# Optimization experiments

Measured on AMD Instinct MI355X. Metric: run time of the kernel, lower is better.

The kernel has to match this reference:

```python
import jax, jax.numpy as jnp
import numpy as np
from jax import lax

EPS = 1e-5

def _conv(x, w, b, stride):
    y = lax.conv_general_dilated(x, w, window_strides=(stride, stride), padding='VALID',
                                 dimension_numbers=('NCHW', 'OIHW', 'NCHW'))
    return y + b[None, :, None, None]

def _upsample_zero(x, s):
    B, C, H, W = x.shape
    z = jnp.zeros((B, C, H * s, W * s), dtype=x.dtype)
    return z.at[:, :, ::s, ::s].set(x)

def setup_inputs() -> dict:
    key = jax.random.key(0)
    ks = jax.random.split(key, 12)
    B, C, H, W = 512, 3, 128, 128
    FLAT = 3 * 65 * 65  # 12675 per the shape chain
    sc = lambda fan_in: 1.0 / np.sqrt(fan_in)
    return {
        'x': jax.random.normal(ks[0], (B, C, H, W), dtype=jnp.float32),
        'bn_gamma': jnp.ones((C,), jnp.float32),
        'bn_beta': jnp.zeros((C,), jnp.float32),
        'w1': jax.random.normal(ks[1], (3, 3, 5, 5), jnp.float32) * sc(3 * 25),
        'b1': jax.random.normal(ks[2], (3,), jnp.float32) * 0.01,
        'w2': jax.random.normal(ks[3], (3, 3, 5, 5), jnp.float32) * sc(3 * 25),
        'b2': jax.random.normal(ks[4], (3,), jnp.float32) * 0.01,
        'fc1_w': jax.random.normal(ks[5], (128, FLAT), jnp.float32) * sc(FLAT),
        'fc1_b': jnp.zeros((128,), jnp.float32),
        'fc2_w': jax.random.normal(ks[6], (10, 128), jnp.float32) * sc(128),
        'fc2_b': jnpp if False else jnp.zeros((10,), jnp.float32),
    }

def reference(x, bn_gamma, bn_beta, w1, b1, w2, b2, fc1_w, fc1_b, fc2_w, fc2_b):
    # BatchNorm1d over active sites (= all original pixels; zero-pad sites are inactive)
    mean = x.mean(axis=(0, 2, 3))
    var = ((x - mean[None, :, None, None]) ** 2).mean(axis=(0, 2, 3))  # biased, as torch BN
    xn = (x - mean[None, :, None, None]) * lax.rsqrt(var + EPS)[None, :, None, None]
    xn = xn * bn_gamma[None, :, None, None] + bn_beta[None, :, None, None]
    # SparseZeroPad2d(1) -> [B,3,130,130]
    h = jnp.pad(xn, ((0, 0), (0, 0), (1, 1), (1, 1)))
    # cv1 (k5,s5) -> [B,3,26,26]; SparseScale2d(5) -> zeros interleaved [B,3,130,130]
    h = _upsample_zero(_conv(h, w1, b1, 5), 5)
    h = jax.nn.relu(h)
    # cv2 (k5,s5) -> [B,3,26,26]; scale -> [B,3,130,130]
    h = _upsample_zero(_conv(h, w2, b2, 5), 5)
    h = jax.nn.relu(h)
    # SparseMaxPool2d(2,2) -> [B,3,65,65]; features >= 0 so dense pool matches sparse pool
    h = lax.reduce_window(h, -jnp.inf, lax.max, (1, 1, 2, 2), (1, 1, 2, 2), 'VALID')
    # flatten -> dropout(eval=identity) -> fc1 -> relu -> fc2 -> log_softmax
    f = h.reshape(h.shape[0], -1)
    f = jax.nn.relu(f @ fc1_w.T + fc1_b)
    logits = f @ fc2_w.T + fc2_b
    return jax.nn.log_softmax(logits, axis=1)
```

## Files before the change

kernel.cpp:

```cpp
#include <hip/hip_runtime.h>

#define BN_EPS 1e-5f

typedef short short8 __attribute__((ext_vector_type(8)));
typedef float f32x4 __attribute__((ext_vector_type(4)));
typedef unsigned short ushort;

__device__ inline ushort f2bf(float f) {
  unsigned int u = __float_as_uint(f);
  u += 0x7FFFu + ((u >> 16) & 1u);
  return (ushort)(u >> 16);
}


#define NPOS 346112
#define LR 136
#define NW 6656

__global__ __launch_bounds__(256) void k_convwave(
    const float* __restrict__ x,
    const float* __restrict__ w1g,
    float* __restrict__ S,
    float* __restrict__ psumA)
{
  __shared__ float lds[4][10 * LR];
  const int tid = threadIdx.x;
  const int lane = tid & 63;
  const int w = tid >> 6;
  float* sx = lds[w];

  const int widx = blockIdx.x * 4 + w;
  const int b = widx / 39;
  const int r39 = widx - b * 39;
  const int c = r39 / 13;
  const int band = r39 - c * 13;
  const int cu = __builtin_amdgcn_readfirstlane(c);

  if (lane < 10) sx[lane * LR + 3] = 0.f;
  else if (lane < 20) sx[(lane - 10) * LR + 132] = 0.f;

  const float* xc = x + ((size_t)b * 3 + c) * 16384;
  const int rbase = 10 * band - 1;
  float s = 0.f, q = 0.f;
  #pragma unroll
  for (int u = 0; u < 5; u++) {
    int v = lane + 64 * u;
    int j = v >> 5;
    int col4 = (v & 31) << 2;
    int r = rbase + j;
    float4 a4 = {0.f, 0.f, 0.f, 0.f};
    if (r >= 0 && r < 128) a4 = *(const float4*)(xc + r * 128 + col4);
    *(float4*)(&sx[j * LR + col4 + 4]) = a4;
    s += (a4.x + a4.y) + (a4.z + a4.w);
    q += (a4.x * a4.x + a4.y * a4.y) + (a4.z * a4.z + a4.w * a4.w);
  }

  const int ol = lane >> 5;
  const int ox = lane & 31;
  if (ox < 26) {
    const float* base = &sx[(5 * ol) * LR + 5 * ox + 3];
    const float* wk = w1g + cu * 25;
    float a0 = 0.f, a1 = 0.f, a2 = 0.f;
    #pragma unroll
    for (int ky = 0; ky < 5; ky++) {
      #pragma unroll
      for (int kx = 0; kx < 5; kx++) {
        float vv = base[ky * LR + kx];
        a0 += wk[ky * 5 + kx] * vv;
        a1 += wk[75 + ky * 5 + kx] * vv;
        a2 += wk[150 + ky * 5 + kx] * vv;
      }
    }
    int oy = 2 * band + ol;
    size_t gp = (size_t)b * 676 + oy * 26 + ox;
    S[(size_t)(c * 3 + 0) * NPOS + gp] = a0;
    S[(size_t)(c * 3 + 1) * NPOS + gp] = a1;
    S[(size_t)(c * 3 + 2) * NPOS + gp] = a2;
  }

  #pragma unroll
  for (int off = 32; off; off >>= 1) {
    s += __shfl_down(s, off);
    q += __shfl_down(q, off);
  }
  if (lane == 0) {
    int pos = b * 13 + band;
    psumA[(size_t)c * NW + pos] = s;
    psumA[(size_t)(3 + c) * NW + pos] = q;
  }
}

__global__ __launch_bounds__(1024) void k_reduce(const float* __restrict__ psumA,
                                                 float* __restrict__ stats) {
  const int sidx = blockIdx.x;
  const float* src = psumA + (size_t)sidx * NW;
  float acc = 0.f;
  for (int i = threadIdx.x; i < NW; i += 1024) acc += src[i];
  #pragma unroll
  for (int off = 32; off; off >>= 1) acc += __shfl_down(acc, off);
  __shared__ float r[16];
  if ((threadIdx.x & 63) == 0) r[threadIdx.x >> 6] = acc;
  __syncthreads();
  if (threadIdx.x == 0) {
    float t = 0.f;
    #pragma unroll
    for (int i = 0; i < 16; i++) t += r[i];
    stats[sidx] = t;
  }
}

__device__ inline float gval(const float* __restrict__ row, int k) {
  if (k >= 2028) return 0.f;
  int c = k / 676;
  int rem = k - c * 676;
  int oy = rem / 26, ox = rem - oy * 26;
  int col = c * 4225 + ((5 * oy) >> 1) * 65 + ((5 * ox) >> 1);
  return row[col];
}

__global__ __launch_bounds__(256) void k_gather(const float* __restrict__ fc1_w,
                                                ushort* __restrict__ WgtB,
                                                ushort* __restrict__ featB) {
  int gid = blockIdx.x * 256 + threadIdx.x;
  if (gid < 10240)
    featB[(size_t)(gid / 20) * 2048 + 2028 + (gid % 20)] = 0;
  int l = gid & 63;
  int n = ((gid >> 12) << 4) + (l & 15);
  int kbase = (((gid >> 6) & 63) << 5) + ((l >> 4) << 3);
  const float* row = fc1_w + n * 12675;
  uint4 o;
  unsigned int w[4];
  #pragma unroll
  for (int i = 0; i < 4; i++) {
    ushort lo = f2bf(gval(row, kbase + 2 * i));
    ushort hi = f2bf(gval(row, kbase + 2 * i + 1));
    w[i] = (unsigned int)lo | ((unsigned int)hi << 16);
  }
  o.x = w[0]; o.y = w[1]; o.z = w[2]; o.w = w[3];
  ((uint4*)WgtB)[gid] = o;
}

__global__ __launch_bounds__(256) void k_combine(
    const float* __restrict__ S,
    const float* __restrict__ stats,
    const float* __restrict__ gamma, const float* __restrict__ beta,
    const float* __restrict__ w1, const float* __restrict__ b1,
    const float* __restrict__ w2, const float* __restrict__ b2,
    ushort* __restrict__ featB)
{
  __shared__ float s_w1[225];
  __shared__ float s_w2[9];
  __shared__ float s_scale[3], s_shift[3], s_b1[3], s_b2[3];
  __shared__ float s_T[9][9];
  const int tid = threadIdx.x;
  if (tid < 225) s_w1[tid] = w1[tid];
  if (tid < 9) s_w2[tid] = w2[tid * 25];
  if (tid < 3) {
    const float N = 512.f * 128.f * 128.f;
    float mean = stats[tid] / N;
    float var = stats[3 + tid] / N - mean * mean;
    float sc = gamma[tid] * rsqrtf(var + BN_EPS);
    s_scale[tid] = sc;
    s_shift[tid] = beta[tid] - mean * sc;
    s_b1[tid] = b1[tid];
    s_b2[tid] = b2[tid];
  }
  __syncthreads();
  if (tid < 81) {
    int cls = tid / 9, oc = tid - (tid / 9) * 9;
    int rcl = cls / 3, ccl = cls - rcl * 3;
    int o = oc / 3, c = oc - o * 3;
    int ky0 = (rcl == 0) ? 1 : 0, ky1 = (rcl == 2) ? 3 : 4;
    int kx0 = (ccl == 0) ? 1 : 0, kx1 = (ccl == 2) ? 3 : 4;
    float t = 0.f;
    for (int ky = ky0; ky <= ky1; ky++)
      for (int kx = kx0; kx <= kx1; kx++)
        t += s_w1[o * 75 + c * 25 + ky * 5 + kx];
    s_T[cls][oc] = t;
  }
  __syncthreads();

  int gpos = blockIdx.x * 256 + tid;
  int b = gpos / 676;
  int pos = gpos - b * 676;
  int oy = pos / 26, ox = pos - oy * 26;
  int rcl = (oy == 0) ? 0 : ((oy == 25) ? 2 : 1);
  int ccl = (ox == 0) ? 0 : ((ox == 25) ? 2 : 1);
  int cls = rcl * 3 + ccl;

  float h[3];
  #pragma unroll
  for (int o = 0; o < 3; o++) {
    float a = s_b1[o];
    #pragma unroll
    for (int c = 0; c < 3; c++) {
      a += s_scale[c] * S[(size_t)(c * 3 + o) * NPOS + gpos];
      a += s_shift[c] * s_T[cls][o * 3 + c];
    }
    h[o] = fmaxf(a, 0.f);
  }
  ushort* fb = featB + (size_t)b * 2048;
  #pragma unroll
  for (int o = 0; o < 3; o++) {
    float v = s_b2[o] + s_w2[3 * o] * h[0] + s_w2[3 * o + 1] * h[1] + s_w2[3 * o + 2] * h[2];
    fb[o * 676 + pos] = f2bf(fmaxf(v, 0.f));
  }
}

__global__ __launch_bounds__(512) void k_fc(
    const ushort* __restrict__ featB,
    const ushort* __restrict__ WgtB,
    const float* __restrict__ fc1_b,
    const float* __restrict__ fc2_w, const float* __restrict__ fc2_b,
    float* __restrict__ out)
{
  __shared__ float s_f[16][132];
  __shared__ float s_lg[16][10];
  const int tid = threadIdx.x;
  const int lane = tid & 63;
  const int t = tid >> 6;
  const int m0 = blockIdx.x * 16;

  const ushort* aptr = featB + (size_t)(m0 + (lane & 15)) * 2048 + ((lane >> 4) << 3);
  const ushort* bptr = WgtB + ((size_t)t * 4096 + lane) * 8;

  f32x4 acc = {0.f, 0.f, 0.f, 0.f};
  #pragma unroll 4
  for (int kk = 0; kk < 64; kk++) {
    short8 a = *(const short8*)(aptr + kk * 32);
    short8 bfr = *(const short8*)(bptr + kk * 512);
    acc = __builtin_amdgcn_mfma_f32_16x16x32_bf16(a, bfr, acc, 0, 0, 0);
  }
  {
    int n = t * 16 + (lane & 15);
    float bias = fc1_b[n];
    int mb = (lane >> 4) << 2;
    #pragma unroll
    for (int r = 0; r < 4; r++)
      s_f[mb + r][n] = fmaxf(acc[r] + bias, 0.f);
  }
  __syncthreads();

  if (tid < 160) {
    int m = tid & 15, q = tid >> 4;
    const float* wr = fc2_w + q * 128;
    float a2 = fc2_b[q];
    #pragma unroll 8
    for (int n = 0; n < 128; n++) a2 += wr[n] * s_f[m][n];
    s_lg[m][q] = a2;
  }
  __syncthreads();

  if (tid < 16) {
    float mx = s_lg[tid][0];
    #pragma unroll
    for (int q = 1; q < 10; q++) mx = fmaxf(mx, s_lg[tid][q]);
    float se = 0.f;
    #pragma unroll
    for (int q = 0; q < 10; q++) se += expf(s_lg[tid][q] - mx);
    float lse = mx + logf(se);
    float* op = out + (size_t)(m0 + tid) * 10;
    #pragma unroll
    for (int q = 0; q < 10; q++) op[q] = s_lg[tid][q] - lse;
  }
}

extern "C" void kernel_launch(void* const* d_in, const int* in_sizes, int n_in,
                              void* d_out, int out_size, void* d_ws, size_t ws_size,
                              hipStream_t stream) {
  const float* x      = (const float*)d_in[0];
  const float* gamma  = (const float*)d_in[1];
  const float* beta   = (const float*)d_in[2];
  const float* w1     = (const float*)d_in[3];
  const float* b1     = (const float*)d_in[4];
  const float* w2     = (const float*)d_in[5];
  const float* b2     = (const float*)d_in[6];
  const float* fc1_w  = (const float*)d_in[7];
  const float* fc1_b  = (const float*)d_in[8];
  const float* fc2_w  = (const float*)d_in[9];
  const float* fc2_b  = (const float*)d_in[10];
  float* out = (float*)d_out;
  float* wsf = (float*)d_ws;

  float* stats  = wsf;
  float* psumA  = wsf + 64;
  ushort* WgtB  = (ushort*)(wsf + 131072);
  ushort* featB = (ushort*)(wsf + 262144);
  float* S      = wsf + 786432;

  k_convwave<<<4992, 256, 0, stream>>>(x, w1, S, psumA);
  k_gather<<<128, 256, 0, stream>>>(fc1_w, WgtB, featB);
  k_reduce<<<6, 1024, 0, stream>>>(psumA, stats);
  k_combine<<<1352, 256, 0, stream>>>(S, stats, gamma, beta, w1, b1, w2, b2, featB);
  k_fc<<<32, 512, 0, stream>>>(featB, WgtB, fc1_b, fc2_w, fc2_b, out);
}
```

Before: 60.80 us.

## Make conv waves process four bands with register prefetch of the next tile

Each wave of the first convolution kernel now handles four work items strided by the original wave count. While it computes the current item, it loads the next item's input rows into registers. The grid shrinks fourfold to match. The aim is to hide global-load latency on the large input read and to cut launch and wave-startup overhead. The cost is more registers held live for the prefetch and fewer resident waves, which lowers occupancy-based latency hiding.

Result: faster. 58.85 us (-3.2%).

```diff
diff --git a/kernel.cpp b/kernel.cpp
--- a/kernel.cpp
+++ b/kernel.cpp
@@ -16,6 +16,7 @@
 #define NPOS 346112
 #define LR 136
 #define NW 6656
+#define WPG 4992
 
 __global__ __launch_bounds__(256) void k_convwave(
     const float* __restrict__ x,
@@ -29,64 +30,102 @@
   const int w = tid >> 6;
   float* sx = lds[w];
 
-  const int widx = blockIdx.x * 4 + w;
-  const int b = widx / 39;
-  const int r39 = widx - b * 39;
-  const int c = r39 / 13;
-  const int band = r39 - c * 13;
-  const int cu = __builtin_amdgcn_readfirstlane(c);
-
   if (lane < 10) sx[lane * LR + 3] = 0.f;
   else if (lane < 20) sx[(lane - 10) * LR + 132] = 0.f;
 
-  const float* xc = x + ((size_t)b * 3 + c) * 16384;
-  const int rbase = 10 * band - 1;
-  float s = 0.f, q = 0.f;
-  #pragma unroll
-  for (int u = 0; u < 5; u++) {
-    int v = lane + 64 * u;
-    int j = v >> 5;
-    int col4 = (v & 31) << 2;
-    int r = rbase + j;
-    float4 a4 = {0.f, 0.f, 0.f, 0.f};
-    if (r >= 0 && r < 128) a4 = *(const float4*)(xc + r * 128 + col4);
-    *(float4*)(&sx[j * LR + col4 + 4]) = a4;
-    s += (a4.x + a4.y) + (a4.z + a4.w);
-    q += (a4.x * a4.x + a4.y * a4.y) + (a4.z * a4.z + a4.w * a4.w);
-  }
-
-  const int ol = lane >> 5;
-  const int ox = lane & 31;
-  if (ox < 26) {
-    const float* base = &sx[(5 * ol) * LR + 5 * ox + 3];
-    const float* wk = w1g + cu * 25;
-    float a0 = 0.f, a1 = 0.f, a2 = 0.f;
-    #pragma unroll
-    for (int ky = 0; ky < 5; ky++) {
+  const int wave0 = blockIdx.x * 4 + w;
+
+  int widx = wave0;
+  int b = widx / 39;
+  int r39 = widx - b * 39;
+  int c = r39 / 13;
+  int band = r39 - c * 13;
+  float4 pf0, pf1, pf2, pf3, pf4;
+  {
+    const float* xc = x + ((size_t)b * 3 + c) * 16384;
+    int rbase = 10 * band - 1;
+    const float4 z = {0.f, 0.f, 0.f, 0.f};
+    #pragma unroll
+    for (int u5 = 0; u5 < 5; u5++) {
+      int v = lane + 64 * u5;
+      int j = v >> 5, col4 = (v & 31) << 2;
+      int r = rbase + j;
+      float4 a4 = (r >= 0 && r < 128) ? *(const float4*)(xc + r * 128 + col4) : z;
+      if (u5 == 0) pf0 = a4; else if (u5 == 1) pf1 = a4; else if (u5 == 2) pf2 = a4;
+      else if (u5 == 3) pf3 = a4; else pf4 = a4;
+    }
+  }
+
+  #pragma unroll
+  for (int it = 0; it < 4; it++) {
+    const int bC = b, cC = c, bandC = band;
+    float4 c0 = pf0, c1 = pf1, c2 = pf2, c3 = pf3, c4 = pf4;
+
+    if (it < 3) {
+      widx = wave0 + (it + 1) * WPG;
+      b = widx / 39;
+      r39 = widx - b * 39;
+      c = r39 / 13;
+      band = r39 - c * 13;
+      const float* xc = x + ((size_t)b * 3 + c) * 16384;
+      int rbase = 10 * band - 1;
+      const float4 z = {0.f, 0.f, 0.f, 0.f};
       #pragma unroll
-      for (int kx = 0; kx < 5; kx++) {
-        float vv = base[ky * LR + kx];
-        a0 += wk[ky * 5 + kx] * vv;
-        a1 += wk[75 + ky * 5 + kx] * vv;
-        a2 += wk[150 + ky * 5 + kx] * vv;
+      for (int u5 = 0; u5 < 5; u5++) {
+        int v = lane + 64 * u5;
+        int j = v >> 5, col4 = (v & 31) << 2;
+        int r = rbase + j;
+        float4 a4 = (r >= 0 && r < 128) ? *(const float4*)(xc + r * 128 + col4) : z;
+        if (u5 == 0) pf0 = a4; else if (u5 == 1) pf1 = a4; else if (u5 == 2) pf2 = a4;
+        else if (u5 == 3) pf3 = a4; else pf4 = a4;
       }
     }
-    int oy = 2 * band + ol;
-    size_t gp = (size_t)b * 676 + oy * 26 + ox;
-    S[(size_t)(c * 3 + 0) * NPOS + gp] = a0;
-    S[(size_t)(c * 3 + 1) * NPOS + gp] = a1;
-    S[(size_t)(c * 3 + 2) * NPOS + gp] = a2;
-  }
-
-  #pragma unroll
-  for (int off = 32; off; off >>= 1) {
-    s += __shfl_down(s, off);
-    q += __shfl_down(q, off);
-  }
-  if (lane == 0) {
-    int pos = b * 13 + band;
-    psumA[(size_t)c * NW + pos] = s;
-    psumA[(size_t)(3 + c) * NW + pos] = q;
+
+    float s = 0.f, q = 0.f;
+    #pragma unroll
+    for (int u5 = 0; u5 < 5; u5++) {
+      float4 a4 = (u5 == 0) ? c0 : (u5 == 1) ? c1 : (u5 == 2) ? c2 : (u5 == 3) ? c3 : c4;
+      int v = lane + 64 * u5;
+      int j = v >> 5, col4 = (v & 31) << 2;
+      *(float4*)(&sx[j * LR + col4 + 4]) = a4;
+      s += (a4.x + a4.y) + (a4.z + a4.w);
+      q += (a4.x * a4.x + a4.y * a4.y) + (a4.z * a4.z + a4.w * a4.w);
+    }
+
+    const int cu = __builtin_amdgcn_readfirstlane(cC);
+    const int ol = lane >> 5;
+    const int ox = lane & 31;
+    if (ox < 26) {
+      const float* base = &sx[(5 * ol) * LR + 5 * ox + 3];
+      const float* wk = w1g + cu * 25;
+      float a0 = 0.f, a1 = 0.f, a2 = 0.f;
+      #pragma unroll
+      for (int ky = 0; ky < 5; ky++) {
+        #pragma unroll
+        for (int kx = 0; kx < 5; kx++) {
+          float vv = base[ky * LR + kx];
+          a0 += wk[ky * 5 + kx] * vv;
+          a1 += wk[75 + ky * 5 + kx] * vv;
+          a2 += wk[150 + ky * 5 + kx] * vv;
+        }
+      }
+      int oy = 2 * bandC + ol;
+      size_t gp = (size_t)bC * 676 + oy * 26 + ox;
+      S[(size_t)(cC * 3 + 0) * NPOS + gp] = a0;
+      S[(size_t)(cC * 3 + 1) * NPOS + gp] = a1;
+      S[(size_t)(cC * 3 + 2) * NPOS + gp] = a2;
+    }
+
+    #pragma unroll
+    for (int off = 32; off; off >>= 1) {
+      s += __shfl_down(s, off);
+      q += __shfl_down(q, off);
+    }
+    if (lane == 0) {
+      int pos = bC * 13 + bandC;
+      psumA[(size_t)cC * NW + pos] = s;
+      psumA[(size_t)(3 + cC) * NW + pos] = q;
+    }
   }
 }
 
@@ -288,7 +327,7 @@
   ushort* featB = (ushort*)(wsf + 262144);
   float* S      = wsf + 786432;
 
-  k_convwave<<<4992, 256, 0, stream>>>(x, w1, S, psumA);
+  k_convwave<<<1248, 256, 0, stream>>>(x, w1, S, psumA);
   k_gather<<<128, 256, 0, stream>>>(fc1_w, WgtB, featB);
   k_reduce<<<6, 1024, 0, stream>>>(psumA, stats);
   k_combine<<<1352, 256, 0, stream>>>(S, stats, gamma, beta, w1, b1, w2, b2, featB);
```
